# Kernel tuning notes

Hardware: AMD Instinct MI355X
Metric: run time of the kernel (lower is better)

## Reference

```python
import jax, jax.numpy as jnp
import numpy as np

GRID = (128, 128, 128)
CENTER = (0.0, 0.0, 0.0)
SIZE = (400.0, 400.0, 400.0)
KERNEL_WIDTH = float(np.sqrt(3.0 * 3.0 * np.pi))  # ~5.317 (from module source)
SIGMA = KERNEL_WIDTH / 2.0
W = 2  # transverse window half-width in voxels (kernel_width / voxel_size ~ 1.7)
ROTATIONS = {'x': [1, 2, 0], 'y': [0, 2, 1], 'z': [0, 1, 2]}
N_LORS = 200000


def _make_lors(key, n, axis, half):
    # endpoints: main-axis coords pinned to the two FOV faces, transverse uniform
    u = jax.random.uniform(key, (n, 6), minval=-half, maxval=half, dtype=jnp.float32)
    u = u.at[:, axis].set(-half).at[:, axis + 3].set(half)
    return u


def setup_inputs() -> dict:
    key = jax.random.key(0)
    k0, k1, k2, k3 = jax.random.split(key, 4)
    image = jax.random.uniform(k0, GRID, dtype=jnp.float32)
    half = SIZE[0] / 2.0
    return {
        'image': image,
        'xlors': _make_lors(k1, N_LORS, 0, half),
        'ylors': _make_lors(k2, N_LORS, 1, half),
        'zlors': _make_lors(k3, N_LORS, 2, half),
    }


def _project_axis(image, lors, perm):
    # rotate image / geometry so the LOR main axis is the last (slice) axis
    img = jnp.transpose(image, perm)                      # [gx, gy, gz]
    g = [GRID[i] for i in perm]
    c = [CENTER[i] for i in perm]
    s = [SIZE[i] for i in perm]
    dx, dy, dz = s[0] / g[0], s[1] / g[1], s[2] / g[2]
    xmin, ymin, zmin = c[0] - s[0] / 2, c[1] - s[1] / 2, c[2] - s[2] / 2

    p0 = lors[:, jnp.array(perm)]                          # [N,3]
    p1 = lors[:, jnp.array([i + 3 for i in perm])]         # [N,3]
    dvec = p1 - p0
    L = jnp.sqrt(jnp.sum(dvec * dvec, axis=1))             # LOR length
    dzl = dvec[:, 2]
    path = dz * L / jnp.abs(dzl)                           # path length per slice

    di = jnp.arange(-W, W + 1)
    doff = jnp.stack(jnp.meshgrid(di, di, indexing='ij'), -1).reshape(-1, 2)  # [25,2]

    def step(acc, k):
        zc = zmin + (k.astype(jnp.float32) + 0.5) * dz     # slice-plane center
        t = (zc - p0[:, 2]) / dzl                          # [N] line parameter
        xc = p0[:, 0] + t * dvec[:, 0]
        yc = p0[:, 1] + t * dvec[:, 1]
        i0 = jnp.floor((xc - xmin) / dx).astype(jnp.int32)
        j0 = jnp.floor((yc - ymin) / dy).astype(jnp.int32)
        ii = i0[:, None] + doff[None, :, 0]                # [N,25]
        jj = j0[:, None] + doff[None, :, 1]
        xi = xmin + (ii.astype(jnp.float32) + 0.5) * dx
        yj = ymin + (jj.astype(jnp.float32) + 0.5) * dy
        d2 = (xi - xc[:, None]) ** 2 + (yj - yc[:, None]) ** 2
        w = jnp.exp(-d2 / (2.0 * SIGMA * SIGMA))
        w = w * (d2 <= KERNEL_WIDTH * KERNEL_WIDTH).astype(jnp.float32)
        inb = ((ii >= 0) & (ii < g[0]) & (jj >= 0) & (jj < g[1])).astype(jnp.float32)
        valid = ((t >= 0.0) & (t <= 1.0)).astype(jnp.float32)
        sl = jax.lax.dynamic_index_in_dim(img, k, axis=2, keepdims=False)  # [gx,gy]
        vals = sl[jnp.clip(ii, 0, g[0] - 1), jnp.clip(jj, 0, g[1] - 1)]
        contrib = jnp.sum(w * inb * vals, axis=1) * path * valid
        return acc + contrib, None

    acc, _ = jax.lax.scan(step, jnp.zeros(lors.shape[0], jnp.float32), jnp.arange(g[2]))
    return acc


def reference(image, xlors, ylors, zlors):
    px = _project_axis(image, xlors, ROTATIONS['x'])
    py = _project_axis(image, ylors, ROTATIONS['y'])
    pz = _project_axis(image, zlors, ROTATIONS['z'])
    return jnp.stack([px, py, pz])  # [3, N]
```

## Files before the change

kernel.cpp:

```cpp
#include <hip/hip_runtime.h>
#include <math.h>

constexpr float DXC    = 3.125f;
constexpr float INV_DX = 0.32f;
constexpr float XMINC  = -200.0f;
constexpr float KW2    = 9.0f * 3.14159265358979323846f;
constexpr float DXC2   = DXC * DXC;
constexpr float KW2C   = KW2 / DXC2;
constexpr float NEGL2C = -(2.0f / KW2) * 1.4426950408889634f * DXC2;
constexpr float WOFF   = 1.7983f;
constexpr float WMIN   = 0.13533528323661270f;

constexpr int TPB    = 1024;
constexpr int LPB    = 1024;
constexpr int LPT    = 2;
constexpr int KSPLIT = 8;
constexpr int KCH    = 128 / KSPLIT;
constexpr int QTAB   = 1024;

__device__ inline unsigned bf16_rn(float x) {
    unsigned u = __float_as_uint(x);
    return (u + 0x7fffu + ((u >> 16) & 1u)) >> 16;
}
__device__ inline unsigned pk_bf16(float x, float y) {
    return bf16_rn(x) | (bf16_rn(y) << 16);
}
__device__ inline float uaf(unsigned u) { return __uint_as_float(u); }

__global__ __launch_bounds__(256) void prep2_kernel(const float* __restrict__ img,
                                                    ushort* __restrict__ V0, ushort* __restrict__ V1,
                                                    ushort* __restrict__ V2, ushort* __restrict__ S0,
                                                    ushort* __restrict__ S1, ushort* __restrict__ S2) {
    int o = blockIdx.x * 256 + threadIdx.x;
    int c = o & 127, b = (o >> 7) & 127, a = o >> 14;
    float x  = img[o];
    float xn = (c < 127) ? img[o + 1] : 0.0f;
    unsigned h  = bf16_rn(x);
    unsigned hn = bf16_rn(xn);
    V0[o] = (ushort)h;
    S0[o] = (ushort)((c < 127) ? hn : 0u);
    int p1 = (b << 14) | (a << 7) | c;
    V1[p1] = (ushort)h;
    S1[p1] = (ushort)((c < 127) ? hn : 0u);
    V2[o] = (ushort)bf16_rn(img[(b << 14) | (c << 7) | a]);
    S2[o] = (ushort)((c < 127) ? bf16_rn(img[(b << 14) | ((c + 1) << 7) | a]) : 0u);
}

__global__ __launch_bounds__(256) void prep_kernel(const float* __restrict__ img,
                                                   ushort* __restrict__ V0,
                                                   ushort* __restrict__ V1,
                                                   ushort* __restrict__ V2) {
    int o = blockIdx.x * 256 + threadIdx.x;
    float x = img[o];
    unsigned h = bf16_rn(x);
    V0[o] = (ushort)h;
    int c = o & 127, b = (o >> 7) & 127, a = o >> 14;
    V1[(b << 14) | (a << 7) | c] = (ushort)h;
    int j = o & 127, i = (o >> 7) & 127, k = o >> 14;
    V2[o] = (ushort)bf16_rn(img[(i << 14) | (j << 7) | k]);
}

__global__ __launch_bounds__(1024) void zero_kernel(float* __restrict__ out, int m) {
    int i = blockIdx.x * 1024 + threadIdx.x;
    if (i < m) out[i] = 0.0f;
}

__device__ inline void stage_one(const ushort* __restrict__ V, int k, int tid, void* dst) {
    const char* src = (const char*)(V + ((size_t)k << 14));
    char* d = (char*)dst;
    int wbase = (tid >> 6) << 10;
    int lane16 = (tid & 63) << 4;
#pragma unroll
    for (int c = 0; c < 2; ++c) {
        int half = c << 14;
        __builtin_amdgcn_global_load_lds(
            (__attribute__((address_space(1))) void*)(const_cast<char*>(src + half + wbase + lane16)),
            (__attribute__((address_space(3))) void*)(d + half + wbase),
            16, 0, 0);
    }
}

struct WIN { float ea0, ea1, ea2, ea3, eb0, eb1, eb2, eb3; int adw; };
struct LST { float u, v, cu, cv, path; };

template <int AXIS>
__device__ inline LST lor_setup(const float* __restrict__ lors, int lorc, int k0) {
    const float* l = lors + (size_t)lorc * 6;
    float l0 = l[0], l1 = l[1], l2 = l[2], l3 = l[3], l4 = l[4], l5 = l[5];
    float p0x, p0y, p0z, p1x, p1y, p1z;
    if (AXIS == 0)      { p0x = l1; p0y = l2; p0z = l0; p1x = l4; p1y = l5; p1z = l3; }
    else if (AXIS == 1) { p0x = l0; p0y = l2; p0z = l1; p1x = l3; p1y = l5; p1z = l4; }
    else                { p0x = l0; p0y = l1; p0z = l2; p1x = l3; p1y = l4; p1z = l5; }
    float dvx = p1x - p0x, dvy = p1y - p0y, dvz = p1z - p0z;
    float L     = sqrtf(dvx * dvx + dvy * dvy + dvz * dvz);
    float invdz = 1.0f / dvz;
    LST s;
    s.path = DXC * L / fabsf(dvz);
    float dux  = dvx * INV_DX, ux0 = (p0x - XMINC) * INV_DX;
    float dvyS = dvy * INV_DX, vy0 = (p0y - XMINC) * INV_DX;
    float tz0 = -p0z * invdz;
    float dt = DXC * invdz;
    s.cu = dux * dt; s.cv = dvyS * dt;
    float zc0 = fmaf((float)k0, DXC, XMINC + 0.5f * DXC);
    float t0  = fmaf(zc0, invdz, tz0);
    s.u = fmaf(t0, dux, ux0);
    s.v = fmaf(t0, dvyS, vy0);
    return s;
}

__device__ inline WIN mkwin(float u, float v, const float4* wt) {
    WIN w;
    float e0f = fminf(fmaxf(floorf(v - WOFF), 0.0f), 124.0f);
    float i0f = fminf(fmaxf(floorf(u - WOFF), 0.0f), 124.0f);
    int qv = min((int)((v - e0f) * (QTAB / 4.0f)), QTAB - 1);
    int qu = min((int)((u - i0f) * (QTAB / 4.0f)), QTAB - 1);
    float4 eb = wt[qv];
    float4 ea = wt[qu];
    int e0 = (int)e0f, i0 = (int)i0f;
    w.adw = (i0 << 6) + (e0 >> 1) + ((e0 & 1) << 13);
    w.ea0 = ea.x; w.ea1 = ea.y; w.ea2 = ea.z; w.ea3 = ea.w;
    w.eb0 = eb.x; w.eb1 = eb.y; w.eb2 = eb.z; w.eb3 = eb.w;
    return w;
}

__device__ inline float do_slice(const WIN& w, const uint* __restrict__ sl, float acc) {
#pragma unroll
    for (int r = 0; r < 4; ++r) {
        int a = w.adw + (r << 6);
        uint d0 = sl[a], d1 = sl[a + 1];
        float x0 = uaf(d0 << 16), x1 = uaf(d0 & 0xffff0000u);
        float x2 = uaf(d1 << 16), x3 = uaf(d1 & 0xffff0000u);
        float er = (r == 0) ? w.ea0 : (r == 1) ? w.ea1 : (r == 2) ? w.ea2 : w.ea3;
        float p0 = er * w.eb0, p1 = er * w.eb1, p2 = er * w.eb2, p3 = er * w.eb3;
        p0 = (p0 >= WMIN) ? p0 : 0.0f;
        p1 = (p1 >= WMIN) ? p1 : 0.0f;
        p2 = (p2 >= WMIN) ? p2 : 0.0f;
        p3 = (p3 >= WMIN) ? p3 : 0.0f;
        acc = fmaf(p0, x0, acc);
        acc = fmaf(p1, x1, acc);
        acc = fmaf(p2, x2, acc);
        acc = fmaf(p3, x3, acc);
    }
    return acc;
}

template <int AXIS>
__device__ void proj_axis9(uint* sl, float4* wt,
                           const ushort* __restrict__ V, const ushort* __restrict__ S,
                           const float* __restrict__ lors,
                           float* __restrict__ out, int n, int blk, int ks)
{
    const int tid = threadIdx.x;
    int lor0 = blk * (LPT * LPB) + tid;
    int lor1 = lor0 + LPB;
    bool act0 = lor0 < n, act1 = lor1 < n;
    int lc0 = act0 ? lor0 : n - 1;
    int lc1 = act1 ? lor1 : n - 1;

    const int k0 = ks * KCH, k1 = k0 + KCH;
    LST s0 = lor_setup<AXIS>(lors, lc0, k0);
    LST s1 = lor_setup<AXIS>(lors, lc1, k0);
    float acc0 = 0.0f, acc1 = 0.0f;

    stage_one(V, k0, tid, sl);
    stage_one(S, k0, tid, sl + 8192);
    {
        float s = ((float)tid + 0.5f) * (4.0f / (float)QTAB);
        float4 e;
        float o0 = 0.5f - s, o1 = 1.5f - s, o2 = 2.5f - s, o3 = 3.5f - s;
        e.x = exp2f(o0 * o0 * NEGL2C);
        e.y = exp2f(o1 * o1 * NEGL2C);
        e.z = exp2f(o2 * o2 * NEGL2C);
        e.w = exp2f(o3 * o3 * NEGL2C);
        wt[tid] = e;
    }
    __syncthreads();

    WIN w0 = mkwin(s0.u, s0.v, wt);
    WIN w1 = mkwin(s1.u, s1.v, wt);

    for (int k = k0; k < k1; ++k) {
        acc0 = do_slice(w0, sl, acc0);
        acc1 = do_slice(w1, sl, acc1);

        if (k < k1 - 1) {
            s0.u += s0.cu; s0.v += s0.cv;
            s1.u += s1.cu; s1.v += s1.cv;
            __syncthreads();
            stage_one(V, k + 1, tid, sl);
            stage_one(S, k + 1, tid, sl + 8192);
            w0 = mkwin(s0.u, s0.v, wt);
            w1 = mkwin(s1.u, s1.v, wt);
            __syncthreads();
        }
    }

    if (act0) atomicAdd(out + lor0, acc0 * s0.path);
    if (act1) atomicAdd(out + lor1, acc1 * s1.path);
}

__global__ __launch_bounds__(TPB, 2) void proj_fused9(const ushort* __restrict__ V0,
                                                      const ushort* __restrict__ V1,
                                                      const ushort* __restrict__ V2,
                                                      const ushort* __restrict__ S0,
                                                      const ushort* __restrict__ S1,
                                                      const ushort* __restrict__ S2,
                                                      const float* __restrict__ xl,
                                                      const float* __restrict__ yl,
                                                      const float* __restrict__ zl,
                                                      float* __restrict__ out,
                                                      int n, int nblk)
{
    __shared__ uint   sl[16384];
    __shared__ float4 wt[QTAB];
    int per = nblk * KSPLIT;
    int axis = blockIdx.x / per;
    int r = blockIdx.x - axis * per;
    int blk = r >> 3;
    int ks  = r & 7;
    if (axis == 0)      proj_axis9<0>(sl, wt, V0, S0, xl, out, n, blk, ks);
    else if (axis == 1) proj_axis9<1>(sl, wt, V1, S1, yl, out + n, n, blk, ks);
    else                proj_axis9<2>(sl, wt, V2, S2, zl, out + 2 * (size_t)n, n, blk, ks);
}

template <int AXIS>
__device__ inline void stage_issue(const float* __restrict__ img, int k, int tid,
                                   float4 st[4]) {
#pragma unroll
    for (int c = 0; c < 4; ++c) {
        int f4 = tid + TPB * c;
        int fl = f4 << 2;
        if (AXIS == 2) {
            int i = fl >> 7, j = fl & 127;
            const float* p = img + (i << 14) + (j << 7) + k;
            st[c] = make_float4(p[0], p[128], p[256], p[384]);
        } else {
            int off;
            if (AXIS == 1) off = ((fl >> 7) << 14) | (k << 7) | (fl & 127);
            else           off = (k << 14) | fl;
            st[c] = *reinterpret_cast<const float4*>(img + off);
        }
    }
}

__device__ inline void stage_write(const float4 st[4], ushort* slb, int tid) {
    uint* w = reinterpret_cast<uint*>(slb);
#pragma unroll
    for (int c = 0; c < 4; ++c) {
        int f4 = tid + TPB * c;
        w[f4 * 2]     = pk_bf16(st[c].x, st[c].y);
        w[f4 * 2 + 1] = pk_bf16(st[c].z, st[c].w);
    }
}

template <int AXIS, bool PRE>
__device__ void proj_axis7(ushort (*sl)[16384], float4* wtab,
                           const ushort* __restrict__ V,
                           const float*  __restrict__ imgF,
                           const float*  __restrict__ lors,
                           float* __restrict__ out, int n, int blk, int ks)
{
    const int tid = threadIdx.x;
    const int lor = blk * LPB + tid;
    const bool active = lor < n;
    const int lorc = active ? lor : n - 1;

    const int k0 = ks * KCH, k1 = k0 + KCH;
    LST s = lor_setup<AXIS>(lors, lorc, k0);
    float u = s.u, v = s.v, cu = s.cu, cv = s.cv;
    float acc = 0.0f;

    if (PRE) {
        stage_one(V, k0, tid, sl[k0 & 1]);
    } else {
        float4 st[4];
        stage_issue<AXIS>(imgF, k0, tid, st);
        stage_write(st, sl[k0 & 1], tid);
    }
    {
        float sx = ((float)tid + 0.5f) * (4.0f / (float)QTAB);
        float4 e;
        float o0 = 0.5f - sx, o1 = 1.5f - sx, o2 = 2.5f - sx, o3 = 3.5f - sx;
        e.x = exp2f(o0 * o0 * NEGL2C);
        e.y = exp2f(o1 * o1 * NEGL2C);
        e.z = exp2f(o2 * o2 * NEGL2C);
        e.w = exp2f(o3 * o3 * NEGL2C);
        wtab[tid] = e;
    }
    __syncthreads();

    for (int k = k0; k < k1; ++k) {
        const ushort* sbuf = sl[k & 1];
        float4 st2[4];
        if (k < k1 - 1) {
            if (PRE) stage_one(V, k + 1, tid, sl[(k & 1) ^ 1]);
            else     stage_issue<AXIS>(imgF, k + 1, tid, st2);
        }

        float e0f = fminf(fmaxf(floorf(v - WOFF), 0.0f), 124.0f);
        int   e0  = (int)e0f;
        int   qv  = min((int)((v - e0f) * (QTAB / 4.0f)), QTAB - 1);
        float4 eb = wtab[qv];
        float i0f = fminf(fmaxf(floorf(u - WOFF), 0.0f), 124.0f);
        int   i0c = (int)i0f;
        int   qu  = min((int)((u - i0f) * (QTAB / 4.0f)), QTAB - 1);
        float4 ea = wtab[qu];
        float eaa[4] = {ea.x, ea.y, ea.z, ea.w};

        const uint* s32 = reinterpret_cast<const uint*>(sbuf);
        int dwc = e0 >> 1;
        int sh  = (e0 & 1) << 4;
        int rowdw = (i0c << 6) + dwc;
#pragma unroll
        for (int r = 0; r < 4; ++r) {
            const uint* sr = s32 + rowdw + (r << 6);
            uint d0 = sr[0], d1 = sr[1], d2 = sr[2];
            uint p01 = __builtin_amdgcn_alignbit(d1, d0, sh);
            uint p23 = __builtin_amdgcn_alignbit(d2, d1, sh);
            float x0 = uaf(p01 << 16);
            float x1 = uaf(p01 & 0xffff0000u);
            float x2 = uaf(p23 << 16);
            float x3 = uaf(p23 & 0xffff0000u);
            float er = eaa[r];
            float p0 = er * eb.x, p1 = er * eb.y, p2 = er * eb.z, p3 = er * eb.w;
            p0 = (p0 >= WMIN) ? p0 : 0.0f;
            p1 = (p1 >= WMIN) ? p1 : 0.0f;
            p2 = (p2 >= WMIN) ? p2 : 0.0f;
            p3 = (p3 >= WMIN) ? p3 : 0.0f;
            acc = fmaf(p0, x0, acc);
            acc = fmaf(p1, x1, acc);
            acc = fmaf(p2, x2, acc);
            acc = fmaf(p3, x3, acc);
        }

        u += cu; v += cv;

        if (k < k1 - 1) {
            if (!PRE) stage_write(st2, sl[(k & 1) ^ 1], tid);
            __syncthreads();
        }
    }

    if (active) atomicAdd(out + lor, acc * s.path);
}

template <bool PRE>
__global__ __launch_bounds__(TPB, 2) void proj_fused7(const float* __restrict__ img,
                                                      const ushort* __restrict__ V0,
                                                      const ushort* __restrict__ V1,
                                                      const ushort* __restrict__ V2,
                                                      const float* __restrict__ xl,
                                                      const float* __restrict__ yl,
                                                      const float* __restrict__ zl,
                                                      float* __restrict__ out,
                                                      int n, int nblk)
{
    __shared__ ushort sl[2][16384];
    __shared__ float4 wtab[QTAB];
    int per = nblk * KSPLIT;
    int axis = blockIdx.x / per;
    int r = blockIdx.x - axis * per;
    int blk = r >> 3;
    int ks  = r & 7;
    if (axis == 0)      proj_axis7<0, PRE>(sl, wtab, V0, img, xl, out, n, blk, ks);
    else if (axis == 1) proj_axis7<1, PRE>(sl, wtab, V1, img, yl, out + n, n, blk, ks);
    else                proj_axis7<2, PRE>(sl, wtab, V2, img, zl, out + 2 * (size_t)n, n, blk, ks);
}

extern "C" void kernel_launch(void* const* d_in, const int* in_sizes, int n_in,
                              void* d_out, int out_size, void* d_ws, size_t ws_size,
                              hipStream_t stream) {
    const float* img   = (const float*)d_in[0];
    const float* xlors = (const float*)d_in[1];
    const float* ylors = (const float*)d_in[2];
    const float* zlors = (const float*)d_in[3];
    float* out = (float*)d_out;

    int n = in_sizes[1] / 6;
    int m = 3 * n;

    zero_kernel<<<(m + 1023) / 1024, 1024, 0, stream>>>(out, m);

    constexpr size_t VOL = 128 * 128 * 128;

    if (ws_size >= 6 * VOL * sizeof(ushort)) {
        int nblk = (n + LPT * LPB - 1) / (LPT * LPB);
        int grid = 3 * nblk * KSPLIT;
        ushort* V0 = (ushort*)d_ws;
        ushort* V1 = V0 + VOL;  ushort* V2 = V1 + VOL;
        ushort* S0 = V2 + VOL;  ushort* S1 = S0 + VOL;  ushort* S2 = S1 + VOL;
        prep2_kernel<<<VOL / 256, 256, 0, stream>>>(img, V0, V1, V2, S0, S1, S2);
        proj_fused9<<<grid, TPB, 0, stream>>>(V0, V1, V2, S0, S1, S2,
                                              xlors, ylors, zlors, out, n, nblk);
    } else if (ws_size >= 3 * VOL * sizeof(ushort)) {
        int nblk = (n + LPB - 1) / LPB;
        int grid = 3 * nblk * KSPLIT;
        ushort* V0 = (ushort*)d_ws;
        ushort* V1 = V0 + VOL;  ushort* V2 = V1 + VOL;
        prep_kernel<<<VOL / 256, 256, 0, stream>>>(img, V0, V1, V2);
        proj_fused7<true><<<grid, TPB, 0, stream>>>(img, V0, V1, V2,
                                                    xlors, ylors, zlors, out, n, nblk);
    } else {
        int nblk = (n + LPB - 1) / LPB;
        int grid = 3 * nblk * KSPLIT;
        proj_fused7<false><<<grid, TPB, 0, stream>>>(img, nullptr, nullptr, nullptr,
                                                     xlors, ylors, zlors, out, n, nblk);
    }
}
```

Measured before the change: 359.9 us.

## Double-buffer slice staging with single bf16 volume and alignbit unaligned reads

Drops the precomputed shifted-copy volumes (S0..S2) and reads three dwords per row, using alignbit to extract odd-aligned bf16 pairs. The two slice buffers now double-buffer, so the next slice's async global-to-LDS load is issued before computing the current one, removing one barrier per slice. The weight table is halved to 512 entries and launch bounds raised to 8. This cuts prep-kernel work and global traffic, and overlaps loads with compute, at the cost of an extra LDS read and an alignbit per row.

```diff
diff --git a/kernel.cpp b/kernel.cpp
--- a/kernel.cpp
+++ b/kernel.cpp
@@ -6,7 +6,6 @@
 constexpr float XMINC  = -200.0f;
 constexpr float KW2    = 9.0f * 3.14159265358979323846f;
 constexpr float DXC2   = DXC * DXC;
-constexpr float KW2C   = KW2 / DXC2;
 constexpr float NEGL2C = -(2.0f / KW2) * 1.4426950408889634f * DXC2;
 constexpr float WOFF   = 1.7983f;
 constexpr float WMIN   = 0.13533528323661270f;
@@ -16,7 +15,7 @@
 constexpr int LPT    = 2;
 constexpr int KSPLIT = 8;
 constexpr int KCH    = 128 / KSPLIT;
-constexpr int QTAB   = 1024;
+constexpr int QTAB   = 512;
 
 __device__ inline unsigned bf16_rn(float x) {
     unsigned u = __float_as_uint(x);
@@ -26,25 +25,6 @@
     return bf16_rn(x) | (bf16_rn(y) << 16);
 }
 __device__ inline float uaf(unsigned u) { return __uint_as_float(u); }
-
-__global__ __launch_bounds__(256) void prep2_kernel(const float* __restrict__ img,
-                                                    ushort* __restrict__ V0, ushort* __restrict__ V1,
-                                                    ushort* __restrict__ V2, ushort* __restrict__ S0,
-                                                    ushort* __restrict__ S1, ushort* __restrict__ S2) {
-    int o = blockIdx.x * 256 + threadIdx.x;
-    int c = o & 127, b = (o >> 7) & 127, a = o >> 14;
-    float x  = img[o];
-    float xn = (c < 127) ? img[o + 1] : 0.0f;
-    unsigned h  = bf16_rn(x);
-    unsigned hn = bf16_rn(xn);
-    V0[o] = (ushort)h;
-    S0[o] = (ushort)((c < 127) ? hn : 0u);
-    int p1 = (b << 14) | (a << 7) | c;
-    V1[p1] = (ushort)h;
-    S1[p1] = (ushort)((c < 127) ? hn : 0u);
-    V2[o] = (ushort)bf16_rn(img[(b << 14) | (c << 7) | a]);
-    S2[o] = (ushort)((c < 127) ? bf16_rn(img[(b << 14) | ((c + 1) << 7) | a]) : 0u);
-}
 
 __global__ __launch_bounds__(256) void prep_kernel(const float* __restrict__ img,
                                                    ushort* __restrict__ V0,
@@ -80,7 +60,7 @@
     }
 }
 
-struct WIN { float ea0, ea1, ea2, ea3, eb0, eb1, eb2, eb3; int adw; };
+struct WIN { float4 ea, eb; int rowdw, sh; };
 struct LST { float u, v, cu, cv, path; };
 
 template <int AXIS>
@@ -114,24 +94,26 @@
     float i0f = fminf(fmaxf(floorf(u - WOFF), 0.0f), 124.0f);
     int qv = min((int)((v - e0f) * (QTAB / 4.0f)), QTAB - 1);
     int qu = min((int)((u - i0f) * (QTAB / 4.0f)), QTAB - 1);
-    float4 eb = wt[qv];
-    float4 ea = wt[qu];
+    w.eb = wt[qv];
+    w.ea = wt[qu];
     int e0 = (int)e0f, i0 = (int)i0f;
-    w.adw = (i0 << 6) + (e0 >> 1) + ((e0 & 1) << 13);
-    w.ea0 = ea.x; w.ea1 = ea.y; w.ea2 = ea.z; w.ea3 = ea.w;
-    w.eb0 = eb.x; w.eb1 = eb.y; w.eb2 = eb.z; w.eb3 = eb.w;
+    w.sh    = (e0 & 1) << 4;
+    w.rowdw = (i0 << 6) + (e0 >> 1);
     return w;
 }
 
 __device__ inline float do_slice(const WIN& w, const uint* __restrict__ sl, float acc) {
+    float eaa[4] = {w.ea.x, w.ea.y, w.ea.z, w.ea.w};
 #pragma unroll
     for (int r = 0; r < 4; ++r) {
-        int a = w.adw + (r << 6);
-        uint d0 = sl[a], d1 = sl[a + 1];
-        float x0 = uaf(d0 << 16), x1 = uaf(d0 & 0xffff0000u);
-        float x2 = uaf(d1 << 16), x3 = uaf(d1 & 0xffff0000u);
-        float er = (r == 0) ? w.ea0 : (r == 1) ? w.ea1 : (r == 2) ? w.ea2 : w.ea3;
-        float p0 = er * w.eb0, p1 = er * w.eb1, p2 = er * w.eb2, p3 = er * w.eb3;
+        const uint* sr = sl + w.rowdw + (r << 6);
+        uint d0 = sr[0], d1 = sr[1], d2 = sr[2];
+        uint p01 = __builtin_amdgcn_alignbit(d1, d0, w.sh);
+        uint p23 = __builtin_amdgcn_alignbit(d2, d1, w.sh);
+        float x0 = uaf(p01 << 16), x1 = uaf(p01 & 0xffff0000u);
+        float x2 = uaf(p23 << 16), x3 = uaf(p23 & 0xffff0000u);
+        float er = eaa[r];
+        float p0 = er * w.eb.x, p1 = er * w.eb.y, p2 = er * w.eb.z, p3 = er * w.eb.w;
         p0 = (p0 >= WMIN) ? p0 : 0.0f;
         p1 = (p1 >= WMIN) ? p1 : 0.0f;
         p2 = (p2 >= WMIN) ? p2 : 0.0f;
@@ -144,27 +126,8 @@
     return acc;
 }
 
-template <int AXIS>
-__device__ void proj_axis9(uint* sl, float4* wt,
-                           const ushort* __restrict__ V, const ushort* __restrict__ S,
-                           const float* __restrict__ lors,
-                           float* __restrict__ out, int n, int blk, int ks)
-{
-    const int tid = threadIdx.x;
-    int lor0 = blk * (LPT * LPB) + tid;
-    int lor1 = lor0 + LPB;
-    bool act0 = lor0 < n, act1 = lor1 < n;
-    int lc0 = act0 ? lor0 : n - 1;
-    int lc1 = act1 ? lor1 : n - 1;
-
-    const int k0 = ks * KCH, k1 = k0 + KCH;
-    LST s0 = lor_setup<AXIS>(lors, lc0, k0);
-    LST s1 = lor_setup<AXIS>(lors, lc1, k0);
-    float acc0 = 0.0f, acc1 = 0.0f;
-
-    stage_one(V, k0, tid, sl);
-    stage_one(S, k0, tid, sl + 8192);
-    {
+__device__ inline void fill_wtab(float4* wt, int tid) {
+    if (tid < QTAB) {
         float s = ((float)tid + 0.5f) * (4.0f / (float)QTAB);
         float4 e;
         float o0 = 0.5f - s, o1 = 1.5f - s, o2 = 2.5f - s, o3 = 3.5f - s;
@@ -174,21 +137,43 @@
         e.w = exp2f(o3 * o3 * NEGL2C);
         wt[tid] = e;
     }
+}
+
+template <int AXIS>
+__device__ void proj_axis10(uint (*sl)[8192], float4* wt,
+                            const ushort* __restrict__ V,
+                            const float* __restrict__ lors,
+                            float* __restrict__ out, int n, int blk, int ks)
+{
+    const int tid = threadIdx.x;
+    int lor0 = blk * (LPT * LPB) + tid;
+    int lor1 = lor0 + LPB;
+    bool act0 = lor0 < n, act1 = lor1 < n;
+    int lc0 = act0 ? lor0 : n - 1;
+    int lc1 = act1 ? lor1 : n - 1;
+
+    const int k0 = ks * KCH, k1 = k0 + KCH;
+    LST s0 = lor_setup<AXIS>(lors, lc0, k0);
+    LST s1 = lor_setup<AXIS>(lors, lc1, k0);
+    float acc0 = 0.0f, acc1 = 0.0f;
+
+    stage_one(V, k0, tid, sl[k0 & 1]);
+    fill_wtab(wt, tid);
     __syncthreads();
 
     WIN w0 = mkwin(s0.u, s0.v, wt);
     WIN w1 = mkwin(s1.u, s1.v, wt);
 
     for (int k = k0; k < k1; ++k) {
-        acc0 = do_slice(w0, sl, acc0);
-        acc1 = do_slice(w1, sl, acc1);
+        const uint* sbuf = sl[k & 1];
+        if (k < k1 - 1) stage_one(V, k + 1, tid, sl[(k & 1) ^ 1]);
+
+        acc0 = do_slice(w0, sbuf, acc0);
+        acc1 = do_slice(w1, sbuf, acc1);
 
         if (k < k1 - 1) {
             s0.u += s0.cu; s0.v += s0.cv;
             s1.u += s1.cu; s1.v += s1.cv;
-            __syncthreads();
-            stage_one(V, k + 1, tid, sl);
-            stage_one(S, k + 1, tid, sl + 8192);
             w0 = mkwin(s0.u, s0.v, wt);
             w1 = mkwin(s1.u, s1.v, wt);
             __syncthreads();
@@ -199,28 +184,25 @@
     if (act1) atomicAdd(out + lor1, acc1 * s1.path);
 }
 
-__global__ __launch_bounds__(TPB, 2) void proj_fused9(const ushort* __restrict__ V0,
-                                                      const ushort* __restrict__ V1,
-                                                      const ushort* __restrict__ V2,
-                                                      const ushort* __restrict__ S0,
-                                                      const ushort* __restrict__ S1,
-                                                      const ushort* __restrict__ S2,
-                                                      const float* __restrict__ xl,
-                                                      const float* __restrict__ yl,
-                                                      const float* __restrict__ zl,
-                                                      float* __restrict__ out,
-                                                      int n, int nblk)
+__global__ __launch_bounds__(TPB, 8) void proj_fused10(const ushort* __restrict__ V0,
+                                                       const ushort* __restrict__ V1,
+                                                       const ushort* __restrict__ V2,
+                                                       const float* __restrict__ xl,
+                                                       const float* __restrict__ yl,
+                                                       const float* __restrict__ zl,
+                                                       float* __restrict__ out,
+                                                       int n, int nblk)
 {
-    __shared__ uint   sl[16384];
+    __shared__ uint   sl[2][8192];
     __shared__ float4 wt[QTAB];
     int per = nblk * KSPLIT;
     int axis = blockIdx.x / per;
     int r = blockIdx.x - axis * per;
     int blk = r >> 3;
     int ks  = r & 7;
-    if (axis == 0)      proj_axis9<0>(sl, wt, V0, S0, xl, out, n, blk, ks);
-    else if (axis == 1) proj_axis9<1>(sl, wt, V1, S1, yl, out + n, n, blk, ks);
-    else                proj_axis9<2>(sl, wt, V2, S2, zl, out + 2 * (size_t)n, n, blk, ks);
+    if (axis == 0)      proj_axis10<0>(sl, wt, V0, xl, out, n, blk, ks);
+    else if (axis == 1) proj_axis10<1>(sl, wt, V1, yl, out + n, n, blk, ks);
+    else                proj_axis10<2>(sl, wt, V2, zl, out + 2 * (size_t)n, n, blk, ks);
 }
 
 template <int AXIS>
@@ -243,18 +225,17 @@
     }
 }
 
-__device__ inline void stage_write(const float4 st[4], ushort* slb, int tid) {
-    uint* w = reinterpret_cast<uint*>(slb);
+__device__ inline void stage_write(const float4 st[4], uint* slb, int tid) {
 #pragma unroll
     for (int c = 0; c < 4; ++c) {
         int f4 = tid + TPB * c;
-        w[f4 * 2]     = pk_bf16(st[c].x, st[c].y);
-        w[f4 * 2 + 1] = pk_bf16(st[c].z, st[c].w);
+        slb[f4 * 2]     = pk_bf16(st[c].x, st[c].y);
+        slb[f4 * 2 + 1] = pk_bf16(st[c].z, st[c].w);
     }
 }
 
 template <int AXIS, bool PRE>
-__device__ void proj_axis7(ushort (*sl)[16384], float4* wtab,
+__device__ void proj_axis7(uint (*sl)[8192], float4* wtab,
                            const ushort* __restrict__ V,
                            const float*  __restrict__ imgF,
                            const float*  __restrict__ lors,
@@ -267,7 +248,6 @@
 
     const int k0 = ks * KCH, k1 = k0 + KCH;
     LST s = lor_setup<AXIS>(lors, lorc, k0);
-    float u = s.u, v = s.v, cu = s.cu, cv = s.cv;
     float acc = 0.0f;
 
     if (PRE) {
@@ -277,65 +257,24 @@
         stage_issue<AXIS>(imgF, k0, tid, st);
         stage_write(st, sl[k0 & 1], tid);
     }
-    {
-        float sx = ((float)tid + 0.5f) * (4.0f / (float)QTAB);
-        float4 e;
-        float o0 = 0.5f - sx, o1 = 1.5f - sx, o2 = 2.5f - sx, o3 = 3.5f - sx;
-        e.x = exp2f(o0 * o0 * NEGL2C);
-        e.y = exp2f(o1 * o1 * NEGL2C);
-        e.z = exp2f(o2 * o2 * NEGL2C);
-        e.w = exp2f(o3 * o3 * NEGL2C);
-        wtab[tid] = e;
-    }
+    fill_wtab(wtab, tid);
     __syncthreads();
 
+    WIN w = mkwin(s.u, s.v, wtab);
+
     for (int k = k0; k < k1; ++k) {
-        const ushort* sbuf = sl[k & 1];
+        const uint* sbuf = sl[k & 1];
         float4 st2[4];
         if (k < k1 - 1) {
             if (PRE) stage_one(V, k + 1, tid, sl[(k & 1) ^ 1]);
             else     stage_issue<AXIS>(imgF, k + 1, tid, st2);
         }
 
-        float e0f = fminf(fmaxf(floorf(v - WOFF), 0.0f), 124.0f);
-        int   e0  = (int)e0f;
-        int   qv  = min((int)((v - e0f) * (QTAB / 4.0f)), QTAB - 1);
-        float4 eb = wtab[qv];
-        float i0f = fminf(fmaxf(floorf(u - WOFF), 0.0f), 124.0f);
-        int   i0c = (int)i0f;
-        int   qu  = min((int)((u - i0f) * (QTAB / 4.0f)), QTAB - 1);
-        float4 ea = wtab[qu];
-        float eaa[4] = {ea.x, ea.y, ea.z, ea.w};
-
-        const uint* s32 = reinterpret_cast<const uint*>(sbuf);
-        int dwc = e0 >> 1;
-        int sh  = (e0 & 1) << 4;
-        int rowdw = (i0c << 6) + dwc;
-#pragma unroll
-        for (int r = 0; r < 4; ++r) {
-            const uint* sr = s32 + rowdw + (r << 6);
-            uint d0 = sr[0], d1 = sr[1], d2 = sr[2];
-            uint p01 = __builtin_amdgcn_alignbit(d1, d0, sh);
-            uint p23 = __builtin_amdgcn_alignbit(d2, d1, sh);
-            float x0 = uaf(p01 << 16);
-            float x1 = uaf(p01 & 0xffff0000u);
-            float x2 = uaf(p23 << 16);
-            float x3 = uaf(p23 & 0xffff0000u);
-            float er = eaa[r];
-            float p0 = er * eb.x, p1 = er * eb.y, p2 = er * eb.z, p3 = er * eb.w;
-            p0 = (p0 >= WMIN) ? p0 : 0.0f;
-            p1 = (p1 >= WMIN) ? p1 : 0.0f;
-            p2 = (p2 >= WMIN) ? p2 : 0.0f;
-            p3 = (p3 >= WMIN) ? p3 : 0.0f;
-            acc = fmaf(p0, x0, acc);
-            acc = fmaf(p1, x1, acc);
-            acc = fmaf(p2, x2, acc);
-            acc = fmaf(p3, x3, acc);
-        }
-
-        u += cu; v += cv;
+        acc = do_slice(w, sbuf, acc);
 
         if (k < k1 - 1) {
+            s.u += s.cu; s.v += s.cv;
+            w = mkwin(s.u, s.v, wtab);
             if (!PRE) stage_write(st2, sl[(k & 1) ^ 1], tid);
             __syncthreads();
         }
@@ -345,7 +284,7 @@
 }
 
 template <bool PRE>
-__global__ __launch_bounds__(TPB, 2) void proj_fused7(const float* __restrict__ img,
+__global__ __launch_bounds__(TPB, 8) void proj_fused7(const float* __restrict__ img,
                                                       const ushort* __restrict__ V0,
                                                       const ushort* __restrict__ V1,
                                                       const ushort* __restrict__ V2,
@@ -355,7 +294,7 @@
                                                       float* __restrict__ out,
                                                       int n, int nblk)
 {
-    __shared__ ushort sl[2][16384];
+    __shared__ uint   sl[2][8192];
     __shared__ float4 wtab[QTAB];
     int per = nblk * KSPLIT;
     int axis = blockIdx.x / per;
@@ -383,23 +322,14 @@
 
     constexpr size_t VOL = 128 * 128 * 128;
 
-    if (ws_size >= 6 * VOL * sizeof(ushort)) {
+    if (ws_size >= 3 * VOL * sizeof(ushort)) {
         int nblk = (n + LPT * LPB - 1) / (LPT * LPB);
         int grid = 3 * nblk * KSPLIT;
         ushort* V0 = (ushort*)d_ws;
         ushort* V1 = V0 + VOL;  ushort* V2 = V1 + VOL;
-        ushort* S0 = V2 + VOL;  ushort* S1 = S0 + VOL;  ushort* S2 = S1 + VOL;
-        prep2_kernel<<<VOL / 256, 256, 0, stream>>>(img, V0, V1, V2, S0, S1, S2);
-        proj_fused9<<<grid, TPB, 0, stream>>>(V0, V1, V2, S0, S1, S2,
-                                              xlors, ylors, zlors, out, n, nblk);
-    } else if (ws_size >= 3 * VOL * sizeof(ushort)) {
-        int nblk = (n + LPB - 1) / LPB;
-        int grid = 3 * nblk * KSPLIT;
-        ushort* V0 = (ushort*)d_ws;
-        ushort* V1 = V0 + VOL;  ushort* V2 = V1 + VOL;
         prep_kernel<<<VOL / 256, 256, 0, stream>>>(img, V0, V1, V2);
-        proj_fused7<true><<<grid, TPB, 0, stream>>>(img, V0, V1, V2,
-                                                    xlors, ylors, zlors, out, n, nblk);
+        proj_fused10<<<grid, TPB, 0, stream>>>(V0, V1, V2,
+                                               xlors, ylors, zlors, out, n, nblk);
     } else {
         int nblk = (n + LPB - 1) / LPB;
         int grid = 3 * nblk * KSPLIT;
```

After: 767.6 us. +113.3%, slower.
